# Kernel tuning notes

Hardware: AMD Instinct MI355X
Metric: run time of the kernel (lower is better)

Reference implementation:

```python
import jax, jax.numpy as jnp
import numpy as np

N = 100000   # nodes
E = 1600000  # edges (avg degree 16)
H = 128      # hidden
S = 10000    # subgraphs
G = 64       # graphs


def setup_inputs() -> dict:
    key = jax.random.key(0)
    ks = jax.random.split(key, 8)
    def w(k, shape, fan_in):
        return jax.random.normal(k, shape, dtype=jnp.float32) * (1.0 / np.sqrt(fan_in))
    return {
        "x": jnp.ones((N, 1), dtype=jnp.float32),
        "edge_index": jax.random.randint(ks[0], (2, E), 0, N, dtype=jnp.int64),
        "node_to_subgraph": jnp.sort(jax.random.randint(ks[1], (N,), 0, S, dtype=jnp.int64)),
        "subgraph_to_graph": jnp.sort(jax.random.randint(ks[2], (S,), 0, G, dtype=jnp.int64)),
        "conv1_W1": w(ks[3], (1, H), 1),
        "conv1_b1": jnp.zeros((H,), jnp.float32),
        "conv1_W2": w(ks[4], (H, H), H),
        "conv1_b2": jnp.zeros((H,), jnp.float32),
        "convs_W1": w(ks[5], (2, H, H), H),
        "convs_b1": jnp.zeros((2, H), jnp.float32),
        "convs_W2": w(ks[6], (2, H, H), H),
        "convs_b2": jnp.zeros((2, H), jnp.float32),
    }


def _gin_layer(x, src, dst, W1, b1, W2, b2):
    # GINConv, train_eps=False, eps=0: nn((1+0)*x + sum_{j in N(i)} x_j)
    agg = jax.ops.segment_sum(x[src], dst, num_segments=x.shape[0])
    h = jax.nn.relu((x + agg) @ W1 + b1)
    return jax.nn.relu(h @ W2 + b2)


def reference(x, edge_index, node_to_subgraph, subgraph_to_graph,
              conv1_W1, conv1_b1, conv1_W2, conv1_b2,
              convs_W1, convs_b1, convs_W2, convs_b2):
    src, dst = edge_index[0], edge_index[1]
    h = _gin_layer(x, src, dst, conv1_W1, conv1_b1, conv1_W2, conv1_b2)
    for i in range(convs_W1.shape[0]):  # num_layers - 1 = 2 structurally distinct layers
        h = _gin_layer(h, src, dst, convs_W1[i], convs_b1[i], convs_W2[i], convs_b2[i])
    # global_add_pool over node_to_subgraph, then subgraph_to_graph
    h = jax.ops.segment_sum(h, node_to_subgraph, num_segments=S)
    h = jax.ops.segment_sum(h, subgraph_to_graph, num_segments=G)
    return h  # [G, H]
```

## Files before the change

### kernel.cpp

```cpp
#include <hip/hip_runtime.h>

typedef unsigned int u32;
typedef unsigned short u16;
typedef __attribute__((ext_vector_type(8))) short bf16x8;
typedef __attribute__((ext_vector_type(4))) float f32x4;

#define CAP 2560
#define CHUNK 8192
#define GMT 2

__device__ __forceinline__ float bfl(u32 v){ return __uint_as_float(v << 16); }
__device__ __forceinline__ float bfh(u32 v){ return __uint_as_float(v & 0xffff0000u); }
__device__ __forceinline__ u16 f2bf(float f){
    u32 u = __float_as_uint(f);
    u += 0x7fffu + ((u >> 16) & 1u);
    return (u16)(u >> 16);
}
__device__ __forceinline__ u32 pack2(float a, float b){
    u32 ua = __float_as_uint(a); ua += 0x7fffu + ((ua >> 16) & 1u);
    u32 ub = __float_as_uint(b); ub += 0x7fffu + ((ub >> 16) & 1u);
    return (ua >> 16) | (ub & 0xffff0000u);
}


__global__ __launch_bounds__(1024) void bucket_count(const int* __restrict__ dst,
                                                     const int* __restrict__ src,
                                                     int* __restrict__ gcur,
                                                     u32* __restrict__ slots,
                                                     int NBk, int E){
    __shared__ int cnt[800];
    int t = threadIdx.x;
    int e0 = blockIdx.x * CHUNK;
    for (int i = t; i < NBk; i += 1024) cnt[i] = 0;
    __syncthreads();
    #pragma unroll
    for (int k = 0; k < CHUNK / 1024; k++){
        int e = e0 + t + k * 1024;
        if (e < E) atomicAdd(&cnt[dst[e] >> 7], 1);
    }
    __syncthreads();
    for (int i = t; i < NBk; i += 1024){
        int c = cnt[i];
        cnt[i] = c ? atomicAdd(&gcur[i], c) : 0;
    }
    __syncthreads();
    #pragma unroll
    for (int k = 0; k < CHUNK / 1024; k++){
        int e = e0 + t + k * 1024;
        if (e < E){
            int d = dst[e];
            int b = d >> 7;
            int pos = atomicAdd(&cnt[b], 1);
            if (pos < CAP) slots[b * CAP + pos] = ((u32)(d & 127) << 17) | (u32)src[e];
        }
    }
}


__global__ __launch_bounds__(512) void bucket_csr(const int* __restrict__ gcur,
                                                  u32* __restrict__ csr,
                                                  int* __restrict__ starts,
                                                  int* __restrict__ ends,
                                                  const float* __restrict__ x,
                                                  const int* __restrict__ n2s,
                                                  const int* __restrict__ s2g,
                                                  float* __restrict__ sval,
                                                  int* __restrict__ gmap, int N){
    __shared__ u32 ebuf[CAP];
    __shared__ int cnt[128], excl[128], cur[128];
    __shared__ float sacc[128];
    int b = blockIdx.x, t = threadIdx.x;
    int base = b * CAP;
    int sz = gcur[b]; if (sz > CAP) sz = CAP;
    if (t < 128){ cnt[t] = 0; sacc[t] = 0.f; }
    __syncthreads();
    for (int i = t; i < sz; i += 512){
        u32 p = csr[base + i];
        ebuf[i] = p;
        atomicAdd(&cnt[p >> 17], 1);
        atomicAdd(&sacc[p >> 17], x[p & 0x1FFFFu]);
    }
    __syncthreads();
    if (t < 64){
        int c0 = cnt[2 * t], c1 = cnt[2 * t + 1];
        int tot = c0 + c1;
        int incl = tot;
        #pragma unroll
        for (int o = 1; o < 64; o <<= 1){
            int v = __shfl_up(incl, o);
            if (t >= o) incl += v;
        }
        int ex = incl - tot;
        excl[2 * t] = ex;
        excl[2 * t + 1] = ex + c0;
    }
    __syncthreads();
    if (t < 128){
        int node = b * 128 + t;
        if (node < N){
            int st = base + excl[t];
            starts[node] = st;
            ends[node] = st + cnt[t];
            sval[node] = x[node] + sacc[t];
            gmap[node] = s2g[n2s[node]];
        }
        cur[t] = excl[t];
    }
    __syncthreads();
    for (int i = t; i < sz; i += 512){
        u32 p = ebuf[i];
        int dl = p >> 17;
        int r = atomicAdd(&cur[dl], 1);
        csr[base + r] = p & 0x1FFFFu;
    }
}


struct W5 { const float* p[5]; };

__global__ void pack_k(W5 w5, u16* __restrict__ wp,
                       int* __restrict__ gcur, int ngcur,
                       float* __restrict__ outz, int nout){
    int m = blockIdx.x;
    int t = threadIdx.x;
    if (m == 5){
        for (int i = t; i < ngcur; i += 256) gcur[i] = 0;
        return;
    }
    if (m == 6){
        for (int i = t; i < nout; i += 256) outz[i] = 0.f;
        return;
    }
    const float* W = w5.p[m];
    u16* dstp = wp + m * 16384;
    #pragma unroll
    for (int it = 0; it < 8; it++){
        int task = t + 256 * it;
        int n = task & 127, c = task >> 7;
        u16 tmp[8];
        #pragma unroll
        for (int j = 0; j < 8; j++) tmp[j] = f2bf(W[(c * 8 + j) * 128 + n]);
        uint4 val;
        val.x = (u32)tmp[0] | ((u32)tmp[1] << 16);
        val.y = (u32)tmp[2] | ((u32)tmp[3] << 16);
        val.z = (u32)tmp[4] | ((u32)tmp[5] << 16);
        val.w = (u32)tmp[6] | ((u32)tmp[7] << 16);
        *(uint4*)(dstp + n * 128 + ((c ^ ((n >> 3) & 15)) << 3)) = val;
    }
}


__global__ __launch_bounds__(256) void gemm1_fused(const float* __restrict__ sval,
                                                   const float* __restrict__ W1,
                                                   const float* __restrict__ b1,
                                                   const u16* __restrict__ Wp,
                                                   const float* __restrict__ bias,
                                                   u16* __restrict__ Out, int nrows){
    __shared__ uint4 ldsbuf[2048];
    __shared__ float w1s[128], b1s[128];
    u16* lds = (u16*)ldsbuf;
    int t = threadIdx.x;
    const uint4* wsrc = (const uint4*)Wp;
    #pragma unroll
    for (int j = 0; j < 8; j++) ldsbuf[t + 256 * j] = wsrc[t + 256 * j];
    if (t < 128){ w1s[t] = W1[t]; b1s[t] = b1[t]; }
    __syncthreads();

    int wave = t >> 6, lane = t & 63;
    int m = lane & 15, q = lane >> 4;
    int r0 = blockIdx.x * (64 * GMT) + wave * (16 * GMT);

    float sv[GMT];
    #pragma unroll
    for (int mt = 0; mt < GMT; mt++){
        int row = r0 + mt * 16 + m;
        if (row >= nrows) row = nrows - 1;
        sv[mt] = sval[row];
    }

    f32x4 acc[GMT][8];
    #pragma unroll
    for (int a = 0; a < GMT; a++)
        #pragma unroll
        for (int b = 0; b < 8; b++){ f32x4 z = {0.f, 0.f, 0.f, 0.f}; acc[a][b] = z; }

    #pragma unroll
    for (int kt = 0; kt < 4; kt++){
        int c = kt * 4 + q;
        int k0 = kt * 32 + q * 8;
        float wk[8], bk[8];
        #pragma unroll
        for (int j = 0; j < 8; j++){ wk[j] = w1s[k0 + j]; bk[j] = b1s[k0 + j]; }
        bf16x8 bfrag[8];
        #pragma unroll
        for (int nt = 0; nt < 8; nt++){
            int n = m * 8 + nt;
            bfrag[nt] = *(const bf16x8*)(lds + n * 128 + ((c ^ m) << 3));
        }
        #pragma unroll
        for (int mt = 0; mt < GMT; mt++){
            bf16x8 afrag;
            #pragma unroll
            for (int j = 0; j < 8; j++){
                float v = sv[mt] * wk[j] + bk[j];
                v = v > 0.f ? v : 0.f;
                afrag[j] = (short)f2bf(v);
            }
            #pragma unroll
            for (int nt = 0; nt < 8; nt++)
                acc[mt][nt] = __builtin_amdgcn_mfma_f32_16x16x32_bf16(afrag, bfrag[nt], acc[mt][nt], 0, 0, 0);
        }
    }

    float4 bb0 = *(const float4*)(bias + m * 8);
    float4 bb1 = *(const float4*)(bias + m * 8 + 4);
    float bb[8] = {bb0.x, bb0.y, bb0.z, bb0.w, bb1.x, bb1.y, bb1.z, bb1.w};
    #pragma unroll
    for (int mt = 0; mt < GMT; mt++){
        #pragma unroll
        for (int r = 0; r < 4; r++){
            int row = r0 + mt * 16 + q * 4 + r;
            if (row < nrows){
                float v[8];
                #pragma unroll
                for (int j = 0; j < 8; j++){
                    float vv = acc[mt][j][r] + bb[j];
                    v[j] = vv > 0.f ? vv : 0.f;
                }
                uint4 o;
                o.x = pack2(v[0], v[1]);
                o.y = pack2(v[2], v[3]);
                o.z = pack2(v[4], v[5]);
                o.w = pack2(v[6], v[7]);
                *(uint4*)(Out + row * 128 + m * 8) = o;
            }
        }
    }
}


__global__ __launch_bounds__(256) void gemm2_fused(const u16* A,
                                                   const u16* __restrict__ Wp1,
                                                   const u16* __restrict__ Wp2,
                                                   const float* __restrict__ bias1,
                                                   const float* __restrict__ bias2,
                                                   u16* Out, int nrows){
    __shared__ uint4 buf1[2048];
    __shared__ uint4 buf2[2048];
    u16* lds1 = (u16*)buf1;
    u16* lds2 = (u16*)buf2;
    int t = threadIdx.x;
    #pragma unroll
    for (int j = 0; j < 8; j++){
        buf1[t + 256 * j] = ((const uint4*)Wp1)[t + 256 * j];
        buf2[t + 256 * j] = ((const uint4*)Wp2)[t + 256 * j];
    }
    __syncthreads();

    int wave = t >> 6, lane = t & 63;
    int m = lane & 15, q = lane >> 4;
    int rl0 = wave * (16 * GMT);
    int r0 = blockIdx.x * (64 * GMT) + rl0;

    f32x4 acc[GMT][8];
    #pragma unroll
    for (int a = 0; a < GMT; a++)
        #pragma unroll
        for (int b = 0; b < 8; b++){ f32x4 z = {0.f, 0.f, 0.f, 0.f}; acc[a][b] = z; }

    #pragma unroll
    for (int kt = 0; kt < 4; kt++){
        int c = kt * 4 + q;
        bf16x8 bfrag[8];
        #pragma unroll
        for (int nt = 0; nt < 8; nt++){
            int n = m * 8 + nt;
            bfrag[nt] = *(const bf16x8*)(lds1 + n * 128 + ((c ^ m) << 3));
        }
        #pragma unroll
        for (int mt = 0; mt < GMT; mt++){
            int row = r0 + mt * 16 + m;
            if (row >= nrows) row = nrows - 1;
            bf16x8 afrag = *(const bf16x8*)(A + row * 128 + kt * 32 + q * 8);
            #pragma unroll
            for (int nt = 0; nt < 8; nt++)
                acc[mt][nt] = __builtin_amdgcn_mfma_f32_16x16x32_bf16(afrag, bfrag[nt], acc[mt][nt], 0, 0, 0);
        }
    }
    __syncthreads();

    {
        float4 bb0 = *(const float4*)(bias1 + m * 8);
        float4 bb1 = *(const float4*)(bias1 + m * 8 + 4);
        float bb[8] = {bb0.x, bb0.y, bb0.z, bb0.w, bb1.x, bb1.y, bb1.z, bb1.w};
        #pragma unroll
        for (int mt = 0; mt < GMT; mt++){
            #pragma unroll
            for (int r = 0; r < 4; r++){
                int rl = rl0 + mt * 16 + q * 4 + r;
                float v[8];
                #pragma unroll
                for (int j = 0; j < 8; j++){
                    float vv = acc[mt][j][r] + bb[j];
                    v[j] = vv > 0.f ? vv : 0.f;
                }
                uint4 o;
                o.x = pack2(v[0], v[1]);
                o.y = pack2(v[2], v[3]);
                o.z = pack2(v[4], v[5]);
                o.w = pack2(v[6], v[7]);
                *(uint4*)(lds1 + rl * 128 + ((m ^ (rl & 15)) << 3)) = o;
            }
        }
    }
    __syncthreads();

    #pragma unroll
    for (int a = 0; a < GMT; a++)
        #pragma unroll
        for (int b = 0; b < 8; b++){ f32x4 z = {0.f, 0.f, 0.f, 0.f}; acc[a][b] = z; }

    #pragma unroll
    for (int kt = 0; kt < 4; kt++){
        int c = kt * 4 + q;
        bf16x8 bfrag[8];
        #pragma unroll
        for (int nt = 0; nt < 8; nt++){
            int n = m * 8 + nt;
            bfrag[nt] = *(const bf16x8*)(lds2 + n * 128 + ((c ^ m) << 3));
        }
        #pragma unroll
        for (int mt = 0; mt < GMT; mt++){
            int rl = rl0 + mt * 16 + m;
            bf16x8 afrag = *(const bf16x8*)(lds1 + rl * 128 + (((kt * 4 + q) ^ (rl & 15)) << 3));
            #pragma unroll
            for (int nt = 0; nt < 8; nt++)
                acc[mt][nt] = __builtin_amdgcn_mfma_f32_16x16x32_bf16(afrag, bfrag[nt], acc[mt][nt], 0, 0, 0);
        }
    }

    float4 bb0 = *(const float4*)(bias2 + m * 8);
    float4 bb1 = *(const float4*)(bias2 + m * 8 + 4);
    float bb[8] = {bb0.x, bb0.y, bb0.z, bb0.w, bb1.x, bb1.y, bb1.z, bb1.w};
    #pragma unroll
    for (int mt = 0; mt < GMT; mt++){
        #pragma unroll
        for (int r = 0; r < 4; r++){
            int row = r0 + mt * 16 + q * 4 + r;
            if (row < nrows){
                float v[8];
                #pragma unroll
                for (int j = 0; j < 8; j++){
                    float vv = acc[mt][j][r] + bb[j];
                    v[j] = vv > 0.f ? vv : 0.f;
                }
                uint4 o;
                o.x = pack2(v[0], v[1]);
                o.y = pack2(v[2], v[3]);
                o.z = pack2(v[4], v[5]);
                o.w = pack2(v[6], v[7]);
                *(uint4*)(Out + row * 128 + m * 8) = o;
            }
        }
    }
}


__device__ __forceinline__ void acc8(float* a, uint4 u){
    a[0] += bfl(u.x); a[1] += bfh(u.x);
    a[2] += bfl(u.y); a[3] += bfh(u.y);
    a[4] += bfl(u.z); a[5] += bfh(u.z);
    a[6] += bfl(u.w); a[7] += bfh(u.w);
}

__global__ __launch_bounds__(256) void agg_k(const uint4* __restrict__ Hin, uint4* __restrict__ Hout,
                                             const int* __restrict__ starts, const int* __restrict__ ends,
                                             const u32* __restrict__ csr, int N){
    int gtid = blockIdx.x * 256 + threadIdx.x;
    int node = gtid >> 4;
    int c = threadIdx.x & 15;
    if (node >= N) return;

    uint4 v = Hin[node * 16 + c];
    float a[8];
    a[0] = bfl(v.x); a[1] = bfh(v.x);
    a[2] = bfl(v.y); a[3] = bfh(v.y);
    a[4] = bfl(v.z); a[5] = bfh(v.z);
    a[6] = bfl(v.w); a[7] = bfh(v.w);

    int b0 = starts[node], b1 = ends[node];
    int j = b0;
    for (; j + 4 <= b1; j += 4){
        int s0 = csr[j], s1 = csr[j + 1], s2 = csr[j + 2], s3 = csr[j + 3];
        uint4 u0 = Hin[s0 * 16 + c];
        uint4 u1 = Hin[s1 * 16 + c];
        uint4 u2 = Hin[s2 * 16 + c];
        uint4 u3 = Hin[s3 * 16 + c];
        acc8(a, u0); acc8(a, u1); acc8(a, u2); acc8(a, u3);
    }
    for (; j < b1; j++){
        int s = csr[j];
        uint4 u = Hin[s * 16 + c];
        acc8(a, u);
    }

    uint4 o;
    o.x = pack2(a[0], a[1]);
    o.y = pack2(a[2], a[3]);
    o.z = pack2(a[4], a[5]);
    o.w = pack2(a[6], a[7]);
    Hout[node * 16 + c] = o;
}


__global__ __launch_bounds__(256) void pool2_k(const u32* __restrict__ H,
                                               const int* __restrict__ gmap,
                                               float* __restrict__ out, int N){
    int c = threadIdx.x & 63;
    int seg = blockIdx.x * 4 + (threadIdx.x >> 6);
    int start = seg * 64;
    if (start >= N) return;
    int end = start + 64; if (end > N) end = N;
    int g = gmap[start];
    float a0 = 0.f, a1 = 0.f;
    for (int n = start; n < end; n++){
        int gn = gmap[n];
        if (gn != g){
            unsafeAtomicAdd(&out[g * 128 + 2 * c], a0);
            unsafeAtomicAdd(&out[g * 128 + 2 * c + 1], a1);
            a0 = 0.f; a1 = 0.f; g = gn;
        }
        u32 u = H[n * 64 + c];
        a0 += bfl(u);
        a1 += bfh(u);
    }
    unsafeAtomicAdd(&out[g * 128 + 2 * c], a0);
    unsafeAtomicAdd(&out[g * 128 + 2 * c + 1], a1);
}

extern "C" void kernel_launch(void* const* d_in, const int* in_sizes, int n_in,
                              void* d_out, int out_size, void* d_ws, size_t ws_size,
                              hipStream_t stream){
    const float* x    = (const float*)d_in[0];
    const int*   ei   = (const int*)d_in[1];
    const int*   n2s  = (const int*)d_in[2];
    const int*   s2g  = (const int*)d_in[3];
    const float* c1W1 = (const float*)d_in[4];
    const float* c1b1 = (const float*)d_in[5];
    const float* c1W2 = (const float*)d_in[6];
    const float* c1b2 = (const float*)d_in[7];
    const float* cW1  = (const float*)d_in[8];
    const float* cb1  = (const float*)d_in[9];
    const float* cW2  = (const float*)d_in[10];
    const float* cb2  = (const float*)d_in[11];
    float* out = (float*)d_out;

    int N = in_sizes[0];
    int E = in_sizes[1] / 2;
    const int* src = ei;
    const int* dst = ei + E;
    int NBk = (N + 127) / 128;

    char* w = (char*)d_ws;
    size_t off = 0;
    auto al = [&](size_t b){ size_t r = off; off += (b + 255) & ~(size_t)255; return r; };
    int*   gcur   = (int*)(w + al((size_t)NBk * 4));
    int*   starts = (int*)(w + al((size_t)N * 4));
    int*   ends   = (int*)(w + al((size_t)N * 4));
    float* sval   = (float*)(w + al((size_t)N * 4));
    int*   gmap   = (int*)(w + al((size_t)N * 4));
    u32*   csr    = (u32*)(w + al((size_t)NBk * CAP * 4));
    u16*   wp     = (u16*)(w + al((size_t)5 * 16384 * 2));
    u16*   P      = (u16*)(w + al((size_t)N * 128 * 2));
    u16*   Q      = (u16*)(w + al((size_t)N * 128 * 2));

    W5 w5;
    w5.p[0] = c1W2;
    w5.p[1] = cW1;
    w5.p[2] = cW2;
    w5.p[3] = cW1 + 16384;
    w5.p[4] = cW2 + 16384;
    pack_k<<<7, 256, 0, stream>>>(w5, wp, gcur, NBk, out, out_size);

    bucket_count<<<(E + CHUNK - 1) / CHUNK, 1024, 0, stream>>>(dst, src, gcur, csr, NBk, E);
    bucket_csr<<<NBk, 512, 0, stream>>>(gcur, csr, starts, ends, x, n2s, s2g, sval, gmap, N);

    int gG = (N + 64 * GMT - 1) / (64 * GMT);
    int gA = (N * 16 + 255) / 256;
    gemm1_fused<<<gG, 256, 0, stream>>>(sval, c1W1, c1b1, wp + 0 * 16384, c1b2, P, N);
    agg_k<<<gA, 256, 0, stream>>>((const uint4*)P, (uint4*)Q, starts, ends, csr, N);
    gemm2_fused<<<gG, 256, 0, stream>>>(Q, wp + 1 * 16384, wp + 2 * 16384, cb1, cb2, Q, N);
    agg_k<<<gA, 256, 0, stream>>>((const uint4*)Q, (uint4*)P, starts, ends, csr, N);
    gemm2_fused<<<gG, 256, 0, stream>>>(P, wp + 3 * 16384, wp + 4 * 16384, cb1 + 128, cb2 + 128, P, N);
    pool2_k<<<(N + 255) / 256, 256, 0, stream>>>((const u32*)P, gmap, out, N);
}
```

Before: 322.4 us.

## Read GEMM weights directly from global memory and sort CSR neighbor lists per node

Measured after the change: 368.0 us. +14.1%, slower.

```diff
diff --git a/kernel.cpp b/kernel.cpp
--- a/kernel.cpp
+++ b/kernel.cpp
@@ -67,6 +67,7 @@
                                                   float* __restrict__ sval,
                                                   int* __restrict__ gmap, int N){
     __shared__ u32 ebuf[CAP];
+    __shared__ u32 lcsr[CAP];
     __shared__ int cnt[128], excl[128], cur[128];
     __shared__ float sacc[128];
     int b = blockIdx.x, t = threadIdx.x;
@@ -111,8 +112,20 @@
         u32 p = ebuf[i];
         int dl = p >> 17;
         int r = atomicAdd(&cur[dl], 1);
-        csr[base + r] = p & 0x1FFFFu;
-    }
+        lcsr[r] = p & 0x1FFFFu;
+    }
+    __syncthreads();
+    if (t < 128){
+        int s0 = excl[t], e0 = s0 + cnt[t];
+        for (int i = s0 + 1; i < e0; i++){
+            u32 key = lcsr[i];
+            int j = i - 1;
+            while (j >= s0 && lcsr[j] > key){ lcsr[j + 1] = lcsr[j]; j--; }
+            lcsr[j + 1] = key;
+        }
+    }
+    __syncthreads();
+    for (int i = t; i < sz; i += 512) csr[base + i] = lcsr[i];
 }
 
 
@@ -156,13 +169,8 @@
                                                    const u16* __restrict__ Wp,
                                                    const float* __restrict__ bias,
                                                    u16* __restrict__ Out, int nrows){
-    __shared__ uint4 ldsbuf[2048];
     __shared__ float w1s[128], b1s[128];
-    u16* lds = (u16*)ldsbuf;
     int t = threadIdx.x;
-    const uint4* wsrc = (const uint4*)Wp;
-    #pragma unroll
-    for (int j = 0; j < 8; j++) ldsbuf[t + 256 * j] = wsrc[t + 256 * j];
     if (t < 128){ w1s[t] = W1[t]; b1s[t] = b1[t]; }
     __syncthreads();
 
@@ -195,7 +203,7 @@
         #pragma unroll
         for (int nt = 0; nt < 8; nt++){
             int n = m * 8 + nt;
-            bfrag[nt] = *(const bf16x8*)(lds + n * 128 + ((c ^ m) << 3));
+            bfrag[nt] = *(const bf16x8*)(Wp + n * 128 + ((c ^ m) << 3));
         }
         #pragma unroll
         for (int mt = 0; mt < GMT; mt++){
@@ -245,17 +253,9 @@
                                                    const float* __restrict__ bias1,
                                                    const float* __restrict__ bias2,
                                                    u16* Out, int nrows){
-    __shared__ uint4 buf1[2048];
-    __shared__ uint4 buf2[2048];
-    u16* lds1 = (u16*)buf1;
-    u16* lds2 = (u16*)buf2;
+    __shared__ uint4 hbuf[2048];
+    u16* lds1 = (u16*)hbuf;
     int t = threadIdx.x;
-    #pragma unroll
-    for (int j = 0; j < 8; j++){
-        buf1[t + 256 * j] = ((const uint4*)Wp1)[t + 256 * j];
-        buf2[t + 256 * j] = ((const uint4*)Wp2)[t + 256 * j];
-    }
-    __syncthreads();
 
     int wave = t >> 6, lane = t & 63;
     int m = lane & 15, q = lane >> 4;
@@ -275,7 +275,7 @@
         #pragma unroll
         for (int nt = 0; nt < 8; nt++){
             int n = m * 8 + nt;
-            bfrag[nt] = *(const bf16x8*)(lds1 + n * 128 + ((c ^ m) << 3));
+            bfrag[nt] = *(const bf16x8*)(Wp1 + n * 128 + ((c ^ m) << 3));
         }
         #pragma unroll
         for (int mt = 0; mt < GMT; mt++){
@@ -287,7 +287,6 @@
                 acc[mt][nt] = __builtin_amdgcn_mfma_f32_16x16x32_bf16(afrag, bfrag[nt], acc[mt][nt], 0, 0, 0);
         }
     }
-    __syncthreads();
 
     {
         float4 bb0 = *(const float4*)(bias1 + m * 8);
@@ -327,7 +326,7 @@
         #pragma unroll
         for (int nt = 0; nt < 8; nt++){
             int n = m * 8 + nt;
-            bfrag[nt] = *(const bf16x8*)(lds2 + n * 128 + ((c ^ m) << 3));
+            bfrag[nt] = *(const bf16x8*)(Wp2 + n * 128 + ((c ^ m) << 3));
         }
         #pragma unroll
         for (int mt = 0; mt < GMT; mt++){
```
